# Optimization experiments

Measured on AMD Instinct MI355X. Metric: run time of the kernel, lower is better.

## Reference

```python
import jax, jax.numpy as jnp
import numpy as np

B, T, D = 16, 512, 512
T_OUT = 2560  # static cap on expanded length (mean total ~2048, +3 sigma << 2560)
MAX_DUR = 8.0


def setup_inputs() -> dict:
    key = jax.random.key(0)
    kx, kd = jax.random.split(key)
    x = jax.random.normal(kx, (B, T, D), dtype=jnp.float32)
    dur = jax.random.uniform(kd, (B, T), dtype=jnp.float32) * MAX_DUR
    return {"x": x, "dur": dur}


def reference(x, dur):
    # Rounded integer durations: (dur + 0.5).long() in torch == floor(dur + 0.5)
    d = jnp.floor(dur + 0.5).astype(jnp.int32)          # [B, T]
    ends = jnp.cumsum(d, axis=1)                         # [B, T] exclusive-end offsets
    pos = jnp.arange(T_OUT, dtype=jnp.int32)             # [T_OUT]
    # For output frame j, source phoneme = first t with ends[t] > j
    src = jax.vmap(lambda e: jnp.searchsorted(e, pos, side='right'))(ends)  # [B, T_OUT]
    src = jnp.minimum(src, x.shape[1] - 1)
    out = jnp.take_along_axis(x, src[:, :, None], axis=1)  # [B, T_OUT, D]
    valid = (pos[None, :] < ends[:, -1:]).astype(x.dtype)  # zero-pad beyond total length
    return out * valid[:, :, None]
```

## Files before the change

kernel.cpp:

```cpp
#include <hip/hip_runtime.h>
#include <math.h>


#define LR_B 16
#define LR_T 512
#define LR_D 512
#define LR_TOUT 2560

__global__ void lr_prep_kernel(const float* __restrict__ dur, int* __restrict__ src) {
    const int b = blockIdx.x;
    const int t = threadIdx.x;
    __shared__ int s[LR_T];
    float dv = dur[b * LR_T + t];
    s[t] = (int)floorf(dv + 0.5f);
    __syncthreads();
    #pragma unroll
    for (int off = 1; off < LR_T; off <<= 1) {
        int v = (t >= off) ? s[t - off] : 0;
        __syncthreads();
        s[t] += v;
        __syncthreads();
    }
    const int total = s[LR_T - 1];
    #pragma unroll
    for (int k = 0; k < LR_TOUT / LR_T; ++k) {
        const int j = t + k * LR_T;
        int v;
        if (j < total) {
            int lo = 0, hi = LR_T;
            #pragma unroll
            for (int it = 0; it < 10; ++it) {
                if (lo < hi) {
                    int mid = (lo + hi) >> 1;
                    if (s[mid] > j) hi = mid; else lo = mid + 1;
                }
            }
            v = (lo < LR_T - 1) ? lo : (LR_T - 1);
        } else {
            v = -1;
        }
        src[b * LR_TOUT + j] = v;
    }
}

__global__ void lr_expand_kernel(const float* __restrict__ x,
                                 const int* __restrict__ src,
                                 float* __restrict__ out) {
    const int b = blockIdx.y;
    const int j = blockIdx.x * 2 + (threadIdx.x >> 7);
    const int lane = threadIdx.x & 127;

    const int si = src[b * LR_TOUT + j];
    float4 val = make_float4(0.f, 0.f, 0.f, 0.f);
    if (si >= 0) {
        const float4* row = (const float4*)(x + (size_t)(b * LR_T + si) * LR_D);
        val = row[lane];
    }
    float4* orow = (float4*)(out + (size_t)(b * LR_TOUT + j) * LR_D);
    orow[lane] = val;
}

extern "C" void kernel_launch(void* const* d_in, const int* in_sizes, int n_in,
                              void* d_out, int out_size, void* d_ws, size_t ws_size,
                              hipStream_t stream) {
    const float* x   = (const float*)d_in[0];
    const float* dur = (const float*)d_in[1];
    float* out = (float*)d_out;
    int* src = (int*)d_ws;

    lr_prep_kernel<<<LR_B, LR_T, 0, stream>>>(dur, src);

    dim3 grid(LR_TOUT / 2, LR_B);
    lr_expand_kernel<<<grid, 256, 0, stream>>>(x, src, out);
}
```

Measured before the change: 107.1 us.

## Fuse duration scan and frame expansion into one kernel with warp-shuffle scan

Merges the prefix-sum/search kernel and the gather kernel into one launch, so the src index array no longer goes through global memory and a second launch with its dependency is avoided. Each block recomputes the full per-batch scan of 512 durations, now using wavefront shuffles plus a small cross-wave pass instead of a shared-memory Hillis-Steele loop with many barriers. Each block then expands 16 output frames. The cost is redundant scan work in every block (160 blocks per batch) and a serialized prologue before each block's copy traffic starts.

```diff
diff --git a/kernel.cpp b/kernel.cpp
--- a/kernel.cpp
+++ b/kernel.cpp
@@ -6,58 +6,74 @@
 #define LR_T 512
 #define LR_D 512
 #define LR_TOUT 2560
+#define FRAMES_PER_BLOCK 16
 
-__global__ void lr_prep_kernel(const float* __restrict__ dur, int* __restrict__ src) {
-    const int b = blockIdx.x;
-    const int t = threadIdx.x;
+__global__ __launch_bounds__(512) void lr_fused_kernel(
+        const float* __restrict__ x,
+        const float* __restrict__ dur,
+        float* __restrict__ out) {
+    const int b    = blockIdx.y;
+    const int base = blockIdx.x * FRAMES_PER_BLOCK;
+    const int tid  = threadIdx.x;
+    const int lane = tid & 63;
+    const int w    = tid >> 6;
+
     __shared__ int s[LR_T];
-    float dv = dur[b * LR_T + t];
-    s[t] = (int)floorf(dv + 0.5f);
+    __shared__ int wsum[8];
+    __shared__ int src16[FRAMES_PER_BLOCK];
+
+    int v = (int)floorf(dur[b * LR_T + tid] + 0.5f);
+    #pragma unroll
+    for (int off = 1; off < 64; off <<= 1) {
+        int n = __shfl_up(v, off, 64);
+        if (lane >= off) v += n;
+    }
+    if (lane == 63) wsum[w] = v;
     __syncthreads();
-    #pragma unroll
-    for (int off = 1; off < LR_T; off <<= 1) {
-        int v = (t >= off) ? s[t - off] : 0;
-        __syncthreads();
-        s[t] += v;
-        __syncthreads();
+    if (tid < 8) {
+        int t = wsum[tid];
+        #pragma unroll
+        for (int off = 1; off < 8; off <<= 1) {
+            int n = __shfl_up(t, off, 8);
+            if (tid >= off) t += n;
+        }
+        wsum[tid] = t;
     }
+    __syncthreads();
+    s[tid] = v + (w > 0 ? wsum[w - 1] : 0);
+    __syncthreads();
+
     const int total = s[LR_T - 1];
-    #pragma unroll
-    for (int k = 0; k < LR_TOUT / LR_T; ++k) {
-        const int j = t + k * LR_T;
-        int v;
+
+    if (tid < FRAMES_PER_BLOCK) {
+        const int j = base + tid;
+        int r = -1;
         if (j < total) {
             int lo = 0, hi = LR_T;
-            #pragma unroll
-            for (int it = 0; it < 10; ++it) {
-                if (lo < hi) {
-                    int mid = (lo + hi) >> 1;
-                    if (s[mid] > j) hi = mid; else lo = mid + 1;
-                }
+            while (lo < hi) {
+                int mid = (lo + hi) >> 1;
+                if (s[mid] > j) hi = mid; else lo = mid + 1;
             }
-            v = (lo < LR_T - 1) ? lo : (LR_T - 1);
-        } else {
-            v = -1;
+            r = (lo < LR_T - 1) ? lo : (LR_T - 1);
         }
-        src[b * LR_TOUT + j] = v;
+        src16[tid] = r;
     }
-}
+    __syncthreads();
 
-__global__ void lr_expand_kernel(const float* __restrict__ x,
-                                 const int* __restrict__ src,
-                                 float* __restrict__ out) {
-    const int b = blockIdx.y;
-    const int j = blockIdx.x * 2 + (threadIdx.x >> 7);
-    const int lane = threadIdx.x & 127;
-
-    const int si = src[b * LR_TOUT + j];
-    float4 val = make_float4(0.f, 0.f, 0.f, 0.f);
-    if (si >= 0) {
-        const float4* row = (const float4*)(x + (size_t)(b * LR_T + si) * LR_D);
-        val = row[lane];
+    const int lane128 = tid & 127;
+    const int fgrp    = tid >> 7;
+    #pragma unroll
+    for (int p = 0; p < 4; ++p) {
+        const int fi = p * 4 + fgrp;
+        const int si = src16[fi];
+        float4 val = make_float4(0.f, 0.f, 0.f, 0.f);
+        if (si >= 0) {
+            const float4* row = (const float4*)(x + (size_t)(b * LR_T + si) * LR_D);
+            val = row[lane128];
+        }
+        float4* orow = (float4*)(out + (size_t)(b * LR_TOUT + base + fi) * LR_D);
+        orow[lane128] = val;
     }
-    float4* orow = (float4*)(out + (size_t)(b * LR_TOUT + j) * LR_D);
-    orow[lane] = val;
 }
 
 extern "C" void kernel_launch(void* const* d_in, const int* in_sizes, int n_in,
@@ -66,10 +82,7 @@
     const float* x   = (const float*)d_in[0];
     const float* dur = (const float*)d_in[1];
     float* out = (float*)d_out;
-    int* src = (int*)d_ws;
 
-    lr_prep_kernel<<<LR_B, LR_T, 0, stream>>>(dur, src);
-
-    dim3 grid(LR_TOUT / 2, LR_B);
-    lr_expand_kernel<<<grid, 256, 0, stream>>>(x, src, out);
+    dim3 grid(LR_TOUT / FRAMES_PER_BLOCK, LR_B);
+    lr_fused_kernel<<<grid, 512, 0, stream>>>(x, dur, out);
 }
```

Measured after the change: 101.8 us. 1.05x faster.
